# Optimization experiments

Hardware: AMD Instinct MI355X
Metric: run time of the kernel (lower is better)

## Reference

```python
import jax, jax.numpy as jnp
import numpy as np

N_NODES = 50000
N_EDGES = 800000
DIM_IN = 64
DIM_H = 32
HEADS = 4
NUM_CLASSES = 10
NEG_SLOPE = 0.2  # DGL GATv2Conv default negative_slope


def _gatv2_layer(x, W_src, b_src, W_dst, b_dst, attn, src, dst):
    """DGL GATv2Conv (share_weights=False, eval mode so feat_drop is identity).
    x: [N, F_in]; attn: [H, D]; returns [N, H, D]."""
    N = x.shape[0]
    H, D = attn.shape
    fs = (x @ W_src + b_src).reshape(N, H, D)  # source projection
    fd = (x @ W_dst + b_dst).reshape(N, H, D)  # destination projection
    # per-edge additive attention: leaky_relu(fs[u] + fd[v]) . attn  -> [E, H]
    e = jax.nn.leaky_relu(fs[src] + fd[dst], NEG_SLOPE)  # [E, H, D]
    s = jnp.einsum('ehd,hd->eh', e, attn)  # [E, H]
    # edge softmax over incoming edges of each destination node
    smax = jax.lax.stop_gradient(
        jax.ops.segment_max(s, dst, num_segments=N))  # [N, H]
    es = jnp.exp(s - smax[dst])
    denom = jax.ops.segment_sum(es, dst, num_segments=N)  # [N, H]
    alpha = es / denom[dst]
    # weighted scatter-aggregate of source features
    out = jax.ops.segment_sum(alpha[:, :, None] * fs[src], dst, num_segments=N)
    return out  # [N, H, D]


def setup_inputs() -> dict:
    key = jax.random.key(0)
    ks = jax.random.split(key, 16)
    sc = 0.05
    inp = {
        'g_feats': jax.random.normal(ks[0], (N_NODES, DIM_IN), jnp.float32),
        'edge_src': jax.random.randint(ks[1], (N_EDGES,), 0, N_NODES, jnp.int32),
        'edge_dst': jax.random.randint(ks[2], (N_EDGES,), 0, N_NODES, jnp.int32),
        # input embedding Linear(dim_in, dim_h)
        'W_in': jax.random.normal(ks[3], (DIM_IN, DIM_H), jnp.float32) * sc,
        'b_in': jnp.zeros((DIM_H,), jnp.float32),
        # GATv2 layer 1: Linear(dim_h, heads*dim_h) for src/dst + attn [H, D]
        'W1_src': jax.random.normal(ks[4], (DIM_H, HEADS * DIM_H), jnp.float32) * sc,
        'b1_src': jnp.zeros((HEADS * DIM_H,), jnp.float32),
        'W1_dst': jax.random.normal(ks[5], (DIM_H, HEADS * DIM_H), jnp.float32) * sc,
        'b1_dst': jnp.zeros((HEADS * DIM_H,), jnp.float32),
        'attn1': jax.random.normal(ks[6], (HEADS, DIM_H), jnp.float32) * sc,
        # GATv2 layer 2
        'W2_src': jax.random.normal(ks[7], (DIM_H, HEADS * DIM_H), jnp.float32) * sc,
        'b2_src': jnp.zeros((HEADS * DIM_H,), jnp.float32),
        'W2_dst': jax.random.normal(ks[8], (DIM_H, HEADS * DIM_H), jnp.float32) * sc,
        'b2_dst': jnp.zeros((HEADS * DIM_H,), jnp.float32),
        'attn2': jax.random.normal(ks[9], (HEADS, DIM_H), jnp.float32) * sc,
        # MLP head: Linear(dim_h, dim_h) -> relu -> (dropout: eval) -> Linear(dim_h, num_classes)
        'Wh1': jax.random.normal(ks[10], (DIM_H, DIM_H), jnp.float32) * sc,
        'bh1': jnp.zeros((DIM_H,), jnp.float32),
        'Wh2': jax.random.normal(ks[11], (DIM_H, NUM_CLASSES), jnp.float32) * sc,
        'bh2': jnp.zeros((NUM_CLASSES,), jnp.float32),
    }
    return inp


def reference(g_feats, W_in, b_in,
              W1_src, b1_src, W1_dst, b1_dst, attn1,
              W2_src, b2_src, W2_dst, b2_dst, attn2,
              Wh1, bh1, Wh2, bh2,
              edge_src, edge_dst):
    x = g_feats @ W_in + b_in  # input embedding, [N, dim_h]
    h = _gatv2_layer(x, W1_src, b1_src, W1_dst, b1_dst, attn1, edge_src, edge_dst)
    h = jax.nn.relu(h.mean(axis=1))  # mean over heads -> [N, dim_h]
    h = _gatv2_layer(h, W2_src, b2_src, W2_dst, b2_dst, attn2, edge_src, edge_dst)
    h = h.mean(axis=1)  # [N, dim_h]
    # dgl.readout_nodes(op='mean') over the single graph -> [1, dim_h]
    g = h.mean(axis=0, keepdims=True)
    g = jax.nn.relu(g @ Wh1 + bh1)  # head (dropout inactive in eval)
    logits = g @ Wh2 + bh2
    return jax.nn.softmax(logits, axis=-1)  # [1, num_classes]
```

## Files before the change

### kernel.cpp

```cpp
#include <hip/hip_runtime.h>
#include <hip/hip_bf16.h>

#define N_NODES 50000
#define N_EDGES 800000
#define DIM_IN 64
#define DIM_H 32
#define HEADS 4
#define NCLS 10
#define NEG 0.2f
#define NBUCK 196
#define NPW 25


__global__ void k_bhist(const int* __restrict__ dst, int* __restrict__ bh) {
    __shared__ int lh[NBUCK];
    for (int i = threadIdx.x; i < NBUCK; i += 256) lh[i] = 0;
    __syncthreads();
    int base = blockIdx.x * 1024 + threadIdx.x;
#pragma unroll
    for (int r = 0; r < 4; r++) {
        int e = base + r * 256;
        if (e < N_EDGES) atomicAdd(&lh[dst[e] >> 8], 1);
    }
    __syncthreads();
    for (int i = threadIdx.x; i < NBUCK; i += 256) {
        int c = lh[i];
        if (c) atomicAdd(&bh[i], c);
    }
}

__global__ void k_bscan(const int* __restrict__ bh, int* __restrict__ bbase,
                        int* __restrict__ gcur) {
    __shared__ int s[256];
    int t = threadIdx.x;
    int v = (t < NBUCK) ? bh[t] : 0;
    s[t] = v;
    __syncthreads();
    for (int off = 1; off < 256; off <<= 1) {
        int u = (t >= off) ? s[t - off] : 0;
        __syncthreads();
        s[t] += u;
        __syncthreads();
    }
    int excl = s[t] - v;
    if (t < NBUCK) {
        bbase[t] = excl;
        gcur[t] = excl;
    }
    if (t == 0) bbase[NBUCK] = N_EDGES;
}

__global__ void k_bin(const int* __restrict__ src, const int* __restrict__ dst,
                      int* __restrict__ gcur, unsigned* __restrict__ stage) {
    __shared__ int lh[NBUCK], chunk[NBUCK];
    int t = threadIdx.x;
    for (int i = t; i < NBUCK; i += 256) lh[i] = 0;
    __syncthreads();
    int e0 = blockIdx.x * 4096;
    unsigned pk[16];
    int bk[16];
#pragma unroll
    for (int r = 0; r < 16; r++) {
        int e = e0 + r * 256 + t;
        bool ok = e < N_EDGES;
        int s = ok ? src[e] : 0;
        int d = ok ? dst[e] : 0;
        bk[r] = ok ? (d >> 8) : -1;
        pk[r] = (unsigned)s | ((unsigned)(d & 255) << 16);
        if (ok) atomicAdd(&lh[bk[r]], 1);
    }
    __syncthreads();
    for (int i = t; i < NBUCK; i += 256) {
        int c = lh[i];
        chunk[i] = c ? atomicAdd(&gcur[i], c) : 0;
        lh[i] = 0;
    }
    __syncthreads();
#pragma unroll
    for (int r = 0; r < 16; r++) {
        if (bk[r] >= 0) {
            int lp = atomicAdd(&lh[bk[r]], 1);
            stage[chunk[bk[r]] + lp] = pk[r];
        }
    }
}

__global__ void k_csr(const unsigned* __restrict__ stage, const int* __restrict__ bbase,
                      int* __restrict__ row, int* __restrict__ adj) {
    __shared__ int lcnt[256], lcur[256], sc[256];
    int b = blockIdx.x, t = threadIdx.x;
    int s0 = bbase[b], s1 = bbase[b + 1];
    lcnt[t] = 0;
    __syncthreads();
    for (int i = s0 + t; i < s1; i += 256) atomicAdd(&lcnt[stage[i] >> 16], 1);
    __syncthreads();
    int v = lcnt[t];
    sc[t] = v;
    __syncthreads();
    for (int off = 1; off < 256; off <<= 1) {
        int u = (t >= off) ? sc[t - off] : 0;
        __syncthreads();
        sc[t] += u;
        __syncthreads();
    }
    int excl = sc[t] - v;
    int n = b * 256 + t;
    if (n < N_NODES) row[n] = s0 + excl;
    if (b == NBUCK - 1 && t == 0) row[N_NODES] = N_EDGES;
    lcur[t] = s0 + excl;
    __syncthreads();
    for (int i = s0 + t; i < s1; i += 256) {
        unsigned p = stage[i];
        int pos = atomicAdd(&lcur[p >> 16], 1);
        adj[pos] = (int)(p & 0xFFFFu);
    }
}


__device__ __forceinline__ unsigned short f2bf(float v) {
    unsigned u = __builtin_bit_cast(unsigned, v);
    u += 0x7FFFu + ((u >> 16) & 1u);
    return (unsigned short)(u >> 16);
}
__device__ __forceinline__ float bfLO(unsigned u) {
    return __builtin_bit_cast(float, u << 16);
}
__device__ __forceinline__ float bfHI(unsigned u) {
    return __builtin_bit_cast(float, u & 0xFFFF0000u);
}

__global__ __launch_bounds__(256, 2) void k_fused1(
    const float* __restrict__ gf, const float* __restrict__ W_in,
    const float* __restrict__ b_in, const float* __restrict__ W1s,
    const float* __restrict__ b1s, const float* __restrict__ W1d,
    const float* __restrict__ b1d, unsigned short* __restrict__ fsh,
    float* __restrict__ fd) {
    __shared__ float4 xb[4][2][8];
    int lane = threadIdx.x & 63;
    int wvl = threadIdx.x >> 6;
    int wave = (blockIdx.x * 256 + threadIdx.x) >> 6;
    int c = lane & 31, h = lane >> 5;
    int n0 = wave * NPW;
    if (n0 >= N_NODES) return;
    float wi[32];
#pragma unroll
    for (int k = 0; k < 32; k++) wi[k] = W_in[(h * 32 + k) * DIM_H + c];
    float bc = b_in[c];
    const float4* Wb = (lane < 32) ? (const float4*)W1s : (const float4*)W1d;
    const float4* bb = (lane < 32) ? (const float4*)b1s : (const float4*)b1d;
    float4 w[32];
#pragma unroll
    for (int k = 0; k < 32; k++) w[k] = Wb[k * 32 + c];
    float4 bias = bb[c];
#pragma unroll 2
    for (int i = 0; i < NPW; i++) {
        int nu = __builtin_amdgcn_readfirstlane(n0 + i);
        const float4* gr = (const float4*)(gf + (size_t)nu * DIM_IN + h * 32);
        float a1 = 0.f;
#pragma unroll
        for (int k4 = 0; k4 < 8; k4++) {
            float4 xv = gr[k4];
            a1 += xv.x * wi[k4 * 4 + 0];
            a1 += xv.y * wi[k4 * 4 + 1];
            a1 += xv.z * wi[k4 * 4 + 2];
            a1 += xv.w * wi[k4 * 4 + 3];
        }
        a1 += __shfl_xor(a1, 32, 64);
        if (lane < 32) ((float*)&xb[wvl][i & 1][0])[c] = a1 + bc;
        float4 acc = bias;
#pragma unroll
        for (int k4 = 0; k4 < 8; k4++) {
            float4 xv = xb[wvl][i & 1][k4];
#pragma unroll
            for (int j = 0; j < 4; j++) {
                float xk = (j == 0) ? xv.x : (j == 1) ? xv.y : (j == 2) ? xv.z : xv.w;
                float4 wk = w[k4 * 4 + j];
                acc.x += xk * wk.x;
                acc.y += xk * wk.y;
                acc.z += xk * wk.z;
                acc.w += xk * wk.w;
            }
        }
        if (lane < 32) {
            ushort4 o;
            o.x = f2bf(acc.x);
            o.y = f2bf(acc.y);
            o.z = f2bf(acc.z);
            o.w = f2bf(acc.w);
            *(ushort4*)&fsh[(size_t)nu * 128 + c * 4] = o;
        } else {
            *(float4*)&fd[(size_t)nu * 128 + c * 4] = acc;
        }
    }
}

__global__ __launch_bounds__(256, 2) void k_proj(
    const float* __restrict__ x, const float* __restrict__ Wsrc,
    const float* __restrict__ bsrc, const float* __restrict__ Wdst,
    const float* __restrict__ bdst, unsigned short* __restrict__ fsh,
    float* __restrict__ fd) {
    int lane = threadIdx.x & 63;
    int wave = (blockIdx.x * 256 + threadIdx.x) >> 6;
    int cl = lane & 31;
    int n0 = wave * NPW;
    if (n0 >= N_NODES) return;
    const float4* Wb = (lane < 32) ? (const float4*)Wsrc : (const float4*)Wdst;
    const float4* bb = (lane < 32) ? (const float4*)bsrc : (const float4*)bdst;
    float4 w[32];
#pragma unroll
    for (int k = 0; k < 32; k++) w[k] = Wb[k * 32 + cl];
    float4 bias = bb[cl];
#pragma unroll 2
    for (int i = 0; i < NPW; i++) {
        int nu = __builtin_amdgcn_readfirstlane(n0 + i);
        const float4* xr = (const float4*)(x + (size_t)nu * DIM_H);
        float4 acc = bias;
#pragma unroll
        for (int k4 = 0; k4 < 8; k4++) {
            float4 xv = xr[k4];
#pragma unroll
            for (int j = 0; j < 4; j++) {
                float xk = (j == 0) ? xv.x : (j == 1) ? xv.y : (j == 2) ? xv.z : xv.w;
                float4 wk = w[k4 * 4 + j];
                acc.x += xk * wk.x;
                acc.y += xk * wk.y;
                acc.z += xk * wk.z;
                acc.w += xk * wk.w;
            }
        }
        if (lane < 32) {
            ushort4 o;
            o.x = f2bf(acc.x);
            o.y = f2bf(acc.y);
            o.z = f2bf(acc.z);
            o.w = f2bf(acc.w);
            *(ushort4*)&fsh[(size_t)nu * 128 + cl * 4] = o;
        } else {
            *(float4*)&fd[(size_t)nu * 128 + cl * 4] = acc;
        }
    }
}

__device__ __forceinline__ void edge4(uint4 u, const float* a8, const float* f8d,
                                      float* acc, float& den, bool valid) {
    float f[8];
    f[0] = bfLO(u.x); f[1] = bfHI(u.x);
    f[2] = bfLO(u.y); f[3] = bfHI(u.y);
    f[4] = bfLO(u.z); f[5] = bfHI(u.z);
    f[6] = bfLO(u.w); f[7] = bfHI(u.w);
    float p = 0.f;
#pragma unroll
    for (int j = 0; j < 8; j++) {
        float t = f[j] + f8d[j];
        t = fmaxf(t, NEG * t);
        p += t * a8[j];
    }
    p += __shfl_xor(p, 1, 64);
    p += __shfl_xor(p, 2, 64);
    float w = __expf(p);
    if (!valid) w = 0.f;
    den += w;
#pragma unroll
    for (int j = 0; j < 8; j++) acc[j] += w * f[j];
}

__global__ void k_gather(const unsigned short* __restrict__ fsh,
                         const float* __restrict__ fd, const float* __restrict__ attn,
                         const int* __restrict__ row, const int* __restrict__ adj,
                         float* __restrict__ xout, float* __restrict__ gpart,
                         int mode) {
    __shared__ float bsum[32];
    int tid = threadIdx.x;
    if (mode) {
        if (tid < 32) bsum[tid] = 0.f;
        __syncthreads();
    }
    int wave = tid >> 6;
    int lane = tid & 63;
    int n = blockIdx.x * 4 + wave;
    int sub = lane & 15, eps = lane >> 4;
    unsigned suboff = (unsigned)sub << 4;
    float a8[8], f8d[8];
    {
        const float4* ap = (const float4*)attn + sub * 2;
        float4 t0 = ap[0], t1 = ap[1];
        a8[0] = t0.x; a8[1] = t0.y; a8[2] = t0.z; a8[3] = t0.w;
        a8[4] = t1.x; a8[5] = t1.y; a8[6] = t1.z; a8[7] = t1.w;
        const float4* fp = (const float4*)(fd + (size_t)n * 128) + sub * 2;
        float4 d0 = fp[0], d1 = fp[1];
        f8d[0] = d0.x; f8d[1] = d0.y; f8d[2] = d0.z; f8d[3] = d0.w;
        f8d[4] = d1.x; f8d[5] = d1.y; f8d[6] = d1.z; f8d[7] = d1.w;
    }
    float acc[8] = {0.f, 0.f, 0.f, 0.f, 0.f, 0.f, 0.f, 0.f};
    float den = 0.f;
    int beg = row[n], end = row[n + 1];
    for (int base = beg; base < end; base += 64) {
        int m = end - base;
        if (m > 64) m = 64;
        int myadj = (lane < m) ? adj[base + lane] : 0;
        int j = 0;
        for (; j + 8 <= m; j += 8) {
            unsigned oa = ((unsigned)__shfl(myadj, j + eps, 64) << 8) + suboff;
            unsigned ob = ((unsigned)__shfl(myadj, j + 4 + eps, 64) << 8) + suboff;
            uint4 ua = *(const uint4*)((const char*)fsh + oa);
            uint4 ub = *(const uint4*)((const char*)fsh + ob);
            edge4(ua, a8, f8d, acc, den, true);
            edge4(ub, a8, f8d, acc, den, true);
        }
        for (; j < m; j += 4) {
            int idx = j + eps;
            bool valid = idx < m;
            unsigned o = ((unsigned)__shfl(myadj, valid ? idx : j, 64) << 8) + suboff;
            uint4 u = *(const uint4*)((const char*)fsh + o);
            edge4(u, a8, f8d, acc, den, valid);
        }
    }
    den += __shfl_xor(den, 16, 64);
    den += __shfl_xor(den, 32, 64);
#pragma unroll
    for (int j = 0; j < 8; j++) {
        acc[j] += __shfl_xor(acc[j], 16, 64);
        acc[j] += __shfl_xor(acc[j], 32, 64);
    }
    float inv = den > 0.f ? 1.f / den : 0.f;
    float o[8];
#pragma unroll
    for (int j = 0; j < 8; j++) {
        float v = acc[j] * inv;
        v += __shfl_xor(v, 4, 64);
        v += __shfl_xor(v, 8, 64);
        o[j] = v * 0.25f;
    }
    if (mode == 0) {
        if (lane < 4) {
            float4 lo, hi;
            lo.x = fmaxf(o[0], 0.f); lo.y = fmaxf(o[1], 0.f);
            lo.z = fmaxf(o[2], 0.f); lo.w = fmaxf(o[3], 0.f);
            hi.x = fmaxf(o[4], 0.f); hi.y = fmaxf(o[5], 0.f);
            hi.z = fmaxf(o[6], 0.f); hi.w = fmaxf(o[7], 0.f);
            float4* xp = (float4*)(xout + (size_t)n * 32 + lane * 8);
            xp[0] = lo;
            xp[1] = hi;
        }
    } else {
        if (lane < 4) {
#pragma unroll
            for (int j = 0; j < 8; j++) atomicAdd(&bsum[lane * 8 + j], o[j]);
        }
        __syncthreads();
        if (tid < 32) atomicAdd(&gpart[(blockIdx.x & 63) * 32 + tid], bsum[tid]);
    }
}

__global__ void k_final(const float* __restrict__ gpart, const float* __restrict__ Wh1,
                        const float* __restrict__ bh1, const float* __restrict__ Wh2,
                        const float* __restrict__ bh2, float* __restrict__ out) {
    __shared__ float gv[32], gh[32], lg[16];
    int t = threadIdx.x;
    if (t < 32) {
        float s = 0.f;
        for (int b = 0; b < 64; b++) s += gpart[b * 32 + t];
        gv[t] = s * (1.f / (float)N_NODES);
    }
    __syncthreads();
    if (t < 32) {
        float s = bh1[t];
        for (int d = 0; d < 32; d++) s += gv[d] * Wh1[d * 32 + t];
        gh[t] = s > 0.f ? s : 0.f;
    }
    __syncthreads();
    if (t < NCLS) {
        float s = bh2[t];
        for (int j = 0; j < 32; j++) s += gh[j] * Wh2[j * NCLS + t];
        lg[t] = s;
    }
    __syncthreads();
    if (t == 0) {
        float m = lg[0];
        for (int c = 1; c < NCLS; c++) m = fmaxf(m, lg[c]);
        float ex[NCLS], sum = 0.f;
        for (int c = 0; c < NCLS; c++) {
            ex[c] = __expf(lg[c] - m);
            sum += ex[c];
        }
        float inv = 1.f / sum;
        for (int c = 0; c < NCLS; c++) out[c] = ex[c] * inv;
    }
}

extern "C" void kernel_launch(void* const* d_in, const int* in_sizes, int n_in,
                              void* d_out, int out_size, void* d_ws, size_t ws_size,
                              hipStream_t stream) {
    const float* g_feats = (const float*)d_in[0];
    const int* edge_src = (const int*)d_in[1];
    const int* edge_dst = (const int*)d_in[2];
    const float* W_in = (const float*)d_in[3];
    const float* b_in = (const float*)d_in[4];
    const float* W1_src = (const float*)d_in[5];
    const float* b1_src = (const float*)d_in[6];
    const float* W1_dst = (const float*)d_in[7];
    const float* b1_dst = (const float*)d_in[8];
    const float* attn1 = (const float*)d_in[9];
    const float* W2_src = (const float*)d_in[10];
    const float* b2_src = (const float*)d_in[11];
    const float* W2_dst = (const float*)d_in[12];
    const float* b2_dst = (const float*)d_in[13];
    const float* attn2 = (const float*)d_in[14];
    const float* Wh1 = (const float*)d_in[15];
    const float* bh1 = (const float*)d_in[16];
    const float* Wh2 = (const float*)d_in[17];
    const float* bh2 = (const float*)d_in[18];

    float* x = (float*)d_ws;
    unsigned short* fsh = (unsigned short*)(x + (size_t)N_NODES * 32);
    float* fd = (float*)(fsh + (size_t)N_NODES * 128);
    float* gpart = fd + (size_t)N_NODES * 128;
    int* bh = (int*)(gpart + 64 * 32);
    int* bbase = bh + NBUCK;
    int* gcur = bbase + NBUCK + 1;
    int* row = gcur + NBUCK;
    unsigned* stage = (unsigned*)(row + N_NODES + 1);
    int* adj = (int*)(stage + N_EDGES);

    const int WB = (N_NODES / NPW + 3) / 4;

    hipMemsetAsync(gpart, 0, (64 * 32 + NBUCK) * sizeof(int), stream);

    k_bhist<<<(N_EDGES + 1023) / 1024, 256, 0, stream>>>(edge_dst, bh);
    k_bscan<<<1, 256, 0, stream>>>(bh, bbase, gcur);
    k_bin<<<(N_EDGES + 4095) / 4096, 256, 0, stream>>>(edge_src, edge_dst, gcur, stage);
    k_csr<<<NBUCK, 256, 0, stream>>>(stage, bbase, row, adj);

    k_fused1<<<WB, 256, 0, stream>>>(g_feats, W_in, b_in, W1_src, b1_src, W1_dst,
                                     b1_dst, fsh, fd);
    k_gather<<<N_NODES / 4, 256, 0, stream>>>(fsh, fd, attn1, row, adj, x, gpart, 0);

    k_proj<<<WB, 256, 0, stream>>>(x, W2_src, b2_src, W2_dst, b2_dst, fsh, fd);
    k_gather<<<N_NODES / 4, 256, 0, stream>>>(fsh, fd, attn2, row, adj, x, gpart, 1);

    k_final<<<1, 256, 0, stream>>>(gpart, Wh1, bh1, Wh2, bh2, (float*)d_out);
}
```

Baseline: 198.2 us.

## Store source features in FP8 and destination features in BF16 for gathers

Source projections are now stored as scaled FP8 (4 bytes per 4 channels), destination projections as scaled BF16 instead of FP32, and adjacency indices as 16-bit. The gather decodes with packed FP8-to-FP32 conversions, uses packed float2 math, adds a 16-edge unrolled loop, and replaces exp with exp2 by folding log2e and the scale into attn. The aim is to roughly halve the bytes per random edge gather, which is the dominant memory-bound cost. The risk is lower precision in attention scores and aggregated features from FP8 quantisation.

```diff
diff --git a/kernel.cpp b/kernel.cpp
--- a/kernel.cpp
+++ b/kernel.cpp
@@ -10,6 +10,18 @@
 #define NEG 0.2f
 #define NBUCK 196
 #define NPW 25
+#define FSCALE 16.0f
+#define LOG2E 1.44269504088896f
+
+typedef float floatx2 __attribute__((ext_vector_type(2)));
+
+__device__ __forceinline__ float fast_exp2(float x) {
+#if __has_builtin(__builtin_amdgcn_exp2f)
+    return __builtin_amdgcn_exp2f(x);
+#else
+    return __expf(x * 0.69314718055994531f);
+#endif
+}
 
 
 __global__ void k_bhist(const int* __restrict__ dst, int* __restrict__ bh) {
@@ -86,7 +98,7 @@
 }
 
 __global__ void k_csr(const unsigned* __restrict__ stage, const int* __restrict__ bbase,
-                      int* __restrict__ row, int* __restrict__ adj) {
+                      int* __restrict__ row, unsigned short* __restrict__ adj) {
     __shared__ int lcnt[256], lcur[256], sc[256];
     int b = blockIdx.x, t = threadIdx.x;
     int s0 = bbase[b], s1 = bbase[b + 1];
@@ -112,7 +124,7 @@
     for (int i = s0 + t; i < s1; i += 256) {
         unsigned p = stage[i];
         int pos = atomicAdd(&lcur[p >> 16], 1);
-        adj[pos] = (int)(p & 0xFFFFu);
+        adj[pos] = (unsigned short)(p & 0xFFFFu);
     }
 }
 
@@ -133,8 +145,8 @@
     const float* __restrict__ gf, const float* __restrict__ W_in,
     const float* __restrict__ b_in, const float* __restrict__ W1s,
     const float* __restrict__ b1s, const float* __restrict__ W1d,
-    const float* __restrict__ b1d, unsigned short* __restrict__ fsh,
-    float* __restrict__ fd) {
+    const float* __restrict__ b1d, unsigned char* __restrict__ fsh,
+    unsigned short* __restrict__ fdh) {
     __shared__ float4 xb[4][2][8];
     int lane = threadIdx.x & 63;
     int wvl = threadIdx.x >> 6;
@@ -148,9 +160,13 @@
     float bc = b_in[c];
     const float4* Wb = (lane < 32) ? (const float4*)W1s : (const float4*)W1d;
     const float4* bb = (lane < 32) ? (const float4*)b1s : (const float4*)b1d;
-    float4 w[32];
-#pragma unroll
-    for (int k = 0; k < 32; k++) w[k] = Wb[k * 32 + c];
+    floatx2 wA[32], wB[32];
+#pragma unroll
+    for (int k = 0; k < 32; k++) {
+        float4 wf = Wb[k * 32 + c];
+        wA[k] = {wf.x, wf.y};
+        wB[k] = {wf.z, wf.w};
+    }
     float4 bias = bb[c];
 #pragma unroll 2
     for (int i = 0; i < NPW; i++) {
@@ -167,29 +183,31 @@
         }
         a1 += __shfl_xor(a1, 32, 64);
         if (lane < 32) ((float*)&xb[wvl][i & 1][0])[c] = a1 + bc;
-        float4 acc = bias;
+        floatx2 acc01 = {bias.x, bias.y}, acc23 = {bias.z, bias.w};
 #pragma unroll
         for (int k4 = 0; k4 < 8; k4++) {
             float4 xv = xb[wvl][i & 1][k4];
 #pragma unroll
             for (int j = 0; j < 4; j++) {
                 float xk = (j == 0) ? xv.x : (j == 1) ? xv.y : (j == 2) ? xv.z : xv.w;
-                float4 wk = w[k4 * 4 + j];
-                acc.x += xk * wk.x;
-                acc.y += xk * wk.y;
-                acc.z += xk * wk.z;
-                acc.w += xk * wk.w;
+                floatx2 xx = {xk, xk};
+                acc01 += xx * wA[k4 * 4 + j];
+                acc23 += xx * wB[k4 * 4 + j];
             }
         }
         if (lane < 32) {
+            int pk = __builtin_amdgcn_cvt_pk_fp8_f32(acc01.x * FSCALE, acc01.y * FSCALE,
+                                                     0, false);
+            pk = __builtin_amdgcn_cvt_pk_fp8_f32(acc23.x * FSCALE, acc23.y * FSCALE,
+                                                 pk, true);
+            *(int*)&fsh[(size_t)nu * 128 + c * 4] = pk;
+        } else {
             ushort4 o;
-            o.x = f2bf(acc.x);
-            o.y = f2bf(acc.y);
-            o.z = f2bf(acc.z);
-            o.w = f2bf(acc.w);
-            *(ushort4*)&fsh[(size_t)nu * 128 + c * 4] = o;
-        } else {
-            *(float4*)&fd[(size_t)nu * 128 + c * 4] = acc;
+            o.x = f2bf(acc01.x * FSCALE);
+            o.y = f2bf(acc01.y * FSCALE);
+            o.z = f2bf(acc23.x * FSCALE);
+            o.w = f2bf(acc23.y * FSCALE);
+            *(ushort4*)&fdh[(size_t)nu * 128 + c * 4] = o;
         }
     }
 }
@@ -197,8 +215,8 @@
 __global__ __launch_bounds__(256, 2) void k_proj(
     const float* __restrict__ x, const float* __restrict__ Wsrc,
     const float* __restrict__ bsrc, const float* __restrict__ Wdst,
-    const float* __restrict__ bdst, unsigned short* __restrict__ fsh,
-    float* __restrict__ fd) {
+    const float* __restrict__ bdst, unsigned char* __restrict__ fsh,
+    unsigned short* __restrict__ fdh) {
     int lane = threadIdx.x & 63;
     int wave = (blockIdx.x * 256 + threadIdx.x) >> 6;
     int cl = lane & 31;
@@ -206,67 +224,82 @@
     if (n0 >= N_NODES) return;
     const float4* Wb = (lane < 32) ? (const float4*)Wsrc : (const float4*)Wdst;
     const float4* bb = (lane < 32) ? (const float4*)bsrc : (const float4*)bdst;
-    float4 w[32];
-#pragma unroll
-    for (int k = 0; k < 32; k++) w[k] = Wb[k * 32 + cl];
+    floatx2 wA[32], wB[32];
+#pragma unroll
+    for (int k = 0; k < 32; k++) {
+        float4 wf = Wb[k * 32 + cl];
+        wA[k] = {wf.x, wf.y};
+        wB[k] = {wf.z, wf.w};
+    }
     float4 bias = bb[cl];
 #pragma unroll 2
     for (int i = 0; i < NPW; i++) {
         int nu = __builtin_amdgcn_readfirstlane(n0 + i);
         const float4* xr = (const float4*)(x + (size_t)nu * DIM_H);
-        float4 acc = bias;
+        floatx2 acc01 = {bias.x, bias.y}, acc23 = {bias.z, bias.w};
 #pragma unroll
         for (int k4 = 0; k4 < 8; k4++) {
             float4 xv = xr[k4];
 #pragma unroll
             for (int j = 0; j < 4; j++) {
                 float xk = (j == 0) ? xv.x : (j == 1) ? xv.y : (j == 2) ? xv.z : xv.w;
-                float4 wk = w[k4 * 4 + j];
-                acc.x += xk * wk.x;
-                acc.y += xk * wk.y;
-                acc.z += xk * wk.z;
-                acc.w += xk * wk.w;
+                floatx2 xx = {xk, xk};
+                acc01 += xx * wA[k4 * 4 + j];
+                acc23 += xx * wB[k4 * 4 + j];
             }
         }
         if (lane < 32) {
+            int pk = __builtin_amdgcn_cvt_pk_fp8_f32(acc01.x * FSCALE, acc01.y * FSCALE,
+                                                     0, false);
+            pk = __builtin_amdgcn_cvt_pk_fp8_f32(acc23.x * FSCALE, acc23.y * FSCALE,
+                                                 pk, true);
+            *(int*)&fsh[(size_t)nu * 128 + cl * 4] = pk;
+        } else {
             ushort4 o;
-            o.x = f2bf(acc.x);
-            o.y = f2bf(acc.y);
-            o.z = f2bf(acc.z);
-            o.w = f2bf(acc.w);
-            *(ushort4*)&fsh[(size_t)nu * 128 + cl * 4] = o;
-        } else {
-            *(float4*)&fd[(size_t)nu * 128 + cl * 4] = acc;
-        }
-    }
-}
-
-__device__ __forceinline__ void edge4(uint4 u, const float* a8, const float* f8d,
-                                      float* acc, float& den, bool valid) {
-    float f[8];
-    f[0] = bfLO(u.x); f[1] = bfHI(u.x);
-    f[2] = bfLO(u.y); f[3] = bfHI(u.y);
-    f[4] = bfLO(u.z); f[5] = bfHI(u.z);
-    f[6] = bfLO(u.w); f[7] = bfHI(u.w);
-    float p = 0.f;
-#pragma unroll
-    for (int j = 0; j < 8; j++) {
-        float t = f[j] + f8d[j];
-        t = fmaxf(t, NEG * t);
-        p += t * a8[j];
-    }
+            o.x = f2bf(acc01.x * FSCALE);
+            o.y = f2bf(acc01.y * FSCALE);
+            o.z = f2bf(acc23.x * FSCALE);
+            o.w = f2bf(acc23.y * FSCALE);
+            *(ushort4*)&fdh[(size_t)nu * 128 + cl * 4] = o;
+        }
+    }
+}
+
+__device__ __forceinline__ void quad_acc(uint2 u, const floatx2* fd8,
+                                         const floatx2* a8, floatx2* acc,
+                                         float& den, bool valid) {
+    floatx2 f0 = __builtin_amdgcn_cvt_pk_f32_fp8((int)u.x, false);
+    floatx2 f1 = __builtin_amdgcn_cvt_pk_f32_fp8((int)u.x, true);
+    floatx2 f2 = __builtin_amdgcn_cvt_pk_f32_fp8((int)u.y, false);
+    floatx2 f3 = __builtin_amdgcn_cvt_pk_f32_fp8((int)u.y, true);
+    floatx2 t0 = f0 + fd8[0];
+    floatx2 t1 = f1 + fd8[1];
+    floatx2 t2 = f2 + fd8[2];
+    floatx2 t3 = f3 + fd8[3];
+    floatx2 n0 = t0 * NEG, n1 = t1 * NEG, n2 = t2 * NEG, n3 = t3 * NEG;
+    floatx2 l0, l1, l2, l3;
+    l0.x = fmaxf(t0.x, n0.x); l0.y = fmaxf(t0.y, n0.y);
+    l1.x = fmaxf(t1.x, n1.x); l1.y = fmaxf(t1.y, n1.y);
+    l2.x = fmaxf(t2.x, n2.x); l2.y = fmaxf(t2.y, n2.y);
+    l3.x = fmaxf(t3.x, n3.x); l3.y = fmaxf(t3.y, n3.y);
+    floatx2 d = l0 * a8[0] + l1 * a8[1] + l2 * a8[2] + l3 * a8[3];
+    float p = d.x + d.y;
     p += __shfl_xor(p, 1, 64);
     p += __shfl_xor(p, 2, 64);
-    float w = __expf(p);
+    float w = fast_exp2(p);
     if (!valid) w = 0.f;
     den += w;
-#pragma unroll
-    for (int j = 0; j < 8; j++) acc[j] += w * f[j];
-}
-
-__global__ void k_gather(const unsigned short* __restrict__ fsh,
-                         const float* __restrict__ fd, const float* __restrict__ attn,
-                         const int* __restrict__ row, const int* __restrict__ adj,
+    floatx2 wv = {w, w};
+    acc[0] += wv * f0;
+    acc[1] += wv * f1;
+    acc[2] += wv * f2;
+    acc[3] += wv * f3;
+}
+
+__global__ void k_gather(const unsigned char* __restrict__ fsh,
+                         const unsigned short* __restrict__ fdh,
+                         const float* __restrict__ attn, const int* __restrict__ row,
+                         const unsigned short* __restrict__ adj,
                          float* __restrict__ xout, float* __restrict__ gpart,
                          int mode) {
     __shared__ float bsum[32];
@@ -278,58 +311,78 @@
     int wave = tid >> 6;
     int lane = tid & 63;
     int n = blockIdx.x * 4 + wave;
-    int sub = lane & 15, eps = lane >> 4;
-    unsigned suboff = (unsigned)sub << 4;
-    float a8[8], f8d[8];
+    int sub = lane & 15, eq = lane >> 4;
+    unsigned suboff = (unsigned)sub << 3;
+    const float asc = LOG2E / FSCALE;
+    floatx2 a8[4], fd8[4];
     {
         const float4* ap = (const float4*)attn + sub * 2;
         float4 t0 = ap[0], t1 = ap[1];
-        a8[0] = t0.x; a8[1] = t0.y; a8[2] = t0.z; a8[3] = t0.w;
-        a8[4] = t1.x; a8[5] = t1.y; a8[6] = t1.z; a8[7] = t1.w;
-        const float4* fp = (const float4*)(fd + (size_t)n * 128) + sub * 2;
-        float4 d0 = fp[0], d1 = fp[1];
-        f8d[0] = d0.x; f8d[1] = d0.y; f8d[2] = d0.z; f8d[3] = d0.w;
-        f8d[4] = d1.x; f8d[5] = d1.y; f8d[6] = d1.z; f8d[7] = d1.w;
-    }
-    float acc[8] = {0.f, 0.f, 0.f, 0.f, 0.f, 0.f, 0.f, 0.f};
+        a8[0] = {t0.x * asc, t0.y * asc};
+        a8[1] = {t0.z * asc, t0.w * asc};
+        a8[2] = {t1.x * asc, t1.y * asc};
+        a8[3] = {t1.z * asc, t1.w * asc};
+        uint4 fdu = *(const uint4*)(fdh + (size_t)n * 128 + sub * 8);
+        fd8[0] = {bfLO(fdu.x), bfHI(fdu.x)};
+        fd8[1] = {bfLO(fdu.y), bfHI(fdu.y)};
+        fd8[2] = {bfLO(fdu.z), bfHI(fdu.z)};
+        fd8[3] = {bfLO(fdu.w), bfHI(fdu.w)};
+    }
+    floatx2 acc[4] = {{0.f, 0.f}, {0.f, 0.f}, {0.f, 0.f}, {0.f, 0.f}};
     float den = 0.f;
     int beg = row[n], end = row[n + 1];
     for (int base = beg; base < end; base += 64) {
         int m = end - base;
         if (m > 64) m = 64;
-        int myadj = (lane < m) ? adj[base + lane] : 0;
+        int myadj = (lane < m) ? (int)adj[base + lane] : 0;
         int j = 0;
+        for (; j + 16 <= m; j += 16) {
+            unsigned o0 = ((unsigned)__shfl(myadj, j + 0 + eq, 64) << 7) + suboff;
+            unsigned o1 = ((unsigned)__shfl(myadj, j + 4 + eq, 64) << 7) + suboff;
+            unsigned o2 = ((unsigned)__shfl(myadj, j + 8 + eq, 64) << 7) + suboff;
+            unsigned o3 = ((unsigned)__shfl(myadj, j + 12 + eq, 64) << 7) + suboff;
+            uint2 u0 = *(const uint2*)(fsh + o0);
+            uint2 u1 = *(const uint2*)(fsh + o1);
+            uint2 u2 = *(const uint2*)(fsh + o2);
+            uint2 u3 = *(const uint2*)(fsh + o3);
+            quad_acc(u0, fd8, a8, acc, den, true);
+            quad_acc(u1, fd8, a8, acc, den, true);
+            quad_acc(u2, fd8, a8, acc, den, true);
+            quad_acc(u3, fd8, a8, acc, den, true);
+        }
         for (; j + 8 <= m; j += 8) {
-            unsigned oa = ((unsigned)__shfl(myadj, j + eps, 64) << 8) + suboff;
-            unsigned ob = ((unsigned)__shfl(myadj, j + 4 + eps, 64) << 8) + suboff;
-            uint4 ua = *(const uint4*)((const char*)fsh + oa);
-            uint4 ub = *(const uint4*)((const char*)fsh + ob);
-            edge4(ua, a8, f8d, acc, den, true);
-            edge4(ub, a8, f8d, acc, den, true);
+            unsigned o0 = ((unsigned)__shfl(myadj, j + 0 + eq, 64) << 7) + suboff;
+            unsigned o1 = ((unsigned)__shfl(myadj, j + 4 + eq, 64) << 7) + suboff;
+            uint2 u0 = *(const uint2*)(fsh + o0);
+            uint2 u1 = *(const uint2*)(fsh + o1);
+            quad_acc(u0, fd8, a8, acc, den, true);
+            quad_acc(u1, fd8, a8, acc, den, true);
         }
         for (; j < m; j += 4) {
-            int idx = j + eps;
+            int idx = j + eq;
             bool valid = idx < m;
-            unsigned o = ((unsigned)__shfl(myadj, valid ? idx : j, 64) << 8) + suboff;
-            uint4 u = *(const uint4*)((const char*)fsh + o);
-            edge4(u, a8, f8d, acc, den, valid);
+            unsigned o = ((unsigned)__shfl(myadj, valid ? idx : j, 64) << 7) + suboff;
+            uint2 u = *(const uint2*)(fsh + o);
+            quad_acc(u, fd8, a8, acc, den, valid);
         }
     }
     den += __shfl_xor(den, 16, 64);
     den += __shfl_xor(den, 32, 64);
+    float av[8] = {acc[0].x, acc[0].y, acc[1].x, acc[1].y,
+                   acc[2].x, acc[2].y, acc[3].x, acc[3].y};
 #pragma unroll
     for (int j = 0; j < 8; j++) {
-        acc[j] += __shfl_xor(acc[j], 16, 64);
-        acc[j] += __shfl_xor(acc[j], 32, 64);
-    }
-    float inv = den > 0.f ? 1.f / den : 0.f;
+        av[j] += __shfl_xor(av[j], 16, 64);
+        av[j] += __shfl_xor(av[j], 32, 64);
+    }
+    float inv = den > 0.f ? (0.25f / FSCALE) / den : 0.f;
     float o[8];
 #pragma unroll
     for (int j = 0; j < 8; j++) {
-        float v = acc[j] * inv;
+        float v = av[j] * inv;
         v += __shfl_xor(v, 4, 64);
         v += __shfl_xor(v, 8, 64);
-        o[j] = v * 0.25f;
+        o[j] = v;
     }
     if (mode == 0) {
         if (lane < 4) {
@@ -412,15 +465,15 @@
     const float* bh2 = (const float*)d_in[18];
 
     float* x = (float*)d_ws;
-    unsigned short* fsh = (unsigned short*)(x + (size_t)N_NODES * 32);
-    float* fd = (float*)(fsh + (size_t)N_NODES * 128);
-    float* gpart = fd + (size_t)N_NODES * 128;
+    unsigned char* fsh = (unsigned char*)(x + (size_t)N_NODES * 32);
+    unsigned short* fdh = (unsigned short*)(fsh + (size_t)N_NODES * 128);
+    float* gpart = (float*)(fdh + (size_t)N_NODES * 128);
     int* bh = (int*)(gpart + 64 * 32);
     int* bbase = bh + NBUCK;
     int* gcur = bbase + NBUCK + 1;
     int* row = gcur + NBUCK;
     unsigned* stage = (unsigned*)(row + N_NODES + 1);
-    int* adj = (int*)(stage + N_EDGES);
+    unsigned short* adj = (unsigned short*)(stage + N_EDGES);
 
     const int WB = (N_NODES / NPW + 3) / 4;
 
@@ -432,11 +485,11 @@
     k_csr<<<NBUCK, 256, 0, stream>>>(stage, bbase, row, adj);
 
     k_fused1<<<WB, 256, 0, stream>>>(g_feats, W_in, b_in, W1_src, b1_src, W1_dst,
-                                     b1_dst, fsh, fd);
-    k_gather<<<N_NODES / 4, 256, 0, stream>>>(fsh, fd, attn1, row, adj, x, gpart, 0);
-
-    k_proj<<<WB, 256, 0, stream>>>(x, W2_src, b2_src, W2_dst, b2_dst, fsh, fd);
-    k_gather<<<N_NODES / 4, 256, 0, stream>>>(fsh, fd, attn2, row, adj, x, gpart, 1);
+                                     b1_dst, fsh, fdh);
+    k_gather<<<N_NODES / 4, 256, 0, stream>>>(fsh, fdh, attn1, row, adj, x, gpart, 0);
+
+    k_proj<<<WB, 256, 0, stream>>>(x, W2_src, b2_src, W2_dst, b2_dst, fsh, fdh);
+    k_gather<<<N_NODES / 4, 256, 0, stream>>>(fsh, fdh, attn2, row, adj, x, gpart, 1);
 
     k_final<<<1, 256, 0, stream>>>(gpart, Wh1, bh1, Wh2, bh2, (float*)d_out);
 }
```

Measured after the change: 188.3 us. 1.05x faster.
